# Kernel optimization log

Hardware: AMD Instinct MI355X
Metric: run time of the kernel (lower is better)

Reference implementation:

```python
import jax, jax.numpy as jnp
import numpy as np

D = 128
H = 8
B = 4
L = 2048


def setup_inputs() -> dict:
    key = jax.random.key(0)
    ks = jax.random.split(key, 5)
    s = 1.0 / np.sqrt(D)
    x = jax.random.normal(ks[0], (B, L, D), dtype=jnp.float32)
    Wq = jax.random.normal(ks[1], (D, D * H), dtype=jnp.float32) * s
    Wk = jax.random.normal(ks[2], (D, D * H), dtype=jnp.float32) * s
    Wv = jax.random.normal(ks[3], (D, D * H), dtype=jnp.float32) * s
    Wu = jax.random.normal(ks[4], (D * H, D), dtype=jnp.float32) * (1.0 / np.sqrt(D * H))
    bu = jnp.zeros((D,), dtype=jnp.float32)
    return {"x": x, "Wq": Wq, "Wk": Wk, "Wv": Wv, "Wu": Wu, "bu": bu}


def reference(x, Wq, Wk, Wv, Wu, bu):
    b, l, d = x.shape
    h = H
    # project and split heads: [b, l, h, d] -> [b, h, l, d]
    q = (x @ Wq).reshape(b, l, h, d).transpose(0, 2, 1, 3)
    k = (x @ Wk).reshape(b, l, h, d).transpose(0, 2, 1, 3)
    v = (x @ Wv).reshape(b, l, h, d).transpose(0, 2, 1, 3)
    scores = jnp.einsum("bhqd,bhkd->bhqk", q, k) / jnp.sqrt(jnp.float32(d))
    w = jax.nn.softmax(scores, axis=-1)
    out = jnp.einsum("bhqk,bhkd->bhqd", w, v)  # [b, h, l, d]
    out = out.transpose(0, 2, 1, 3).reshape(b, l, h * d)
    return out @ Wu + bu
```

## Files before the change

### kernel.cpp

```cpp
#include <hip/hip_runtime.h>
#include <stdint.h>

#define D_ 128
#define H_ 8
#define B_ 4
#define L_ 2048
#define NH (B_*H_)

typedef __bf16 bf16x8 __attribute__((ext_vector_type(8)));
typedef float f32x4 __attribute__((ext_vector_type(4)));
typedef float f32x16 __attribute__((ext_vector_type(16)));
typedef unsigned short u16;
typedef u16 u16x2 __attribute__((ext_vector_type(2)));
typedef u16 u16x4 __attribute__((ext_vector_type(4)));
typedef u16 u16x8 __attribute__((ext_vector_type(8)));
typedef uint32_t u32x2 __attribute__((ext_vector_type(2)));
typedef uint32_t u32x4 __attribute__((ext_vector_type(4)));
typedef float fvec4 __attribute__((ext_vector_type(4)));

__device__ __forceinline__ u16 f2b(float f){
    uint32_t u = __builtin_bit_cast(uint32_t, f);
    u += 0x7fffu + ((u >> 16) & 1u);
    return (u16)(u >> 16);
}
__device__ __forceinline__ u16 f2b_native(float f){
    return __builtin_bit_cast(u16, (__bf16)f);
}
__device__ __forceinline__ uint32_t pk2(float a, float b){
    u16x2 v = { f2b_native(a), f2b_native(b) };
    return __builtin_bit_cast(uint32_t, v);
}
__device__ __forceinline__ float ex2(float x){
#if __has_builtin(__builtin_amdgcn_exp2f)
    return __builtin_amdgcn_exp2f(x);
#else
    return exp2f(x);
#endif
}
__device__ __forceinline__ u32x2 permswap(uint32_t a, uint32_t b){
#if __has_builtin(__builtin_amdgcn_permlane32_swap)
    return __builtin_amdgcn_permlane32_swap(a, b, false, false);
#else
    asm volatile("v_permlane32_swap_b32 %0, %1" : "+v"(a), "+v"(b));
    u32x2 r; r[0] = a; r[1] = b; return r;
#endif
}
__device__ __forceinline__ bf16x8 asbf(u16x8 v){ return __builtin_bit_cast(bf16x8, v); }
#define MFMA(a,b,c)   __builtin_amdgcn_mfma_f32_16x16x32_bf16((a),(b),(c),0,0,0)
#define MFMA32(a,b,c) __builtin_amdgcn_mfma_f32_32x32x16_bf16((a),(b),(c),0,0,0)

__device__ __forceinline__ void gld16(const u16* g, u16* l){
    __builtin_amdgcn_global_load_lds(
        (const __attribute__((address_space(1))) void*)g,
        (__attribute__((address_space(3))) void*)l, 16, 0, 0);
}

__global__ __launch_bounds__(256)
void cvt_all(const float* __restrict__ x, const float* __restrict__ Wq,
             const float* __restrict__ Wk, const float* __restrict__ Wv,
             const float* __restrict__ Wu,
             u16* __restrict__ xb, u16* __restrict__ wT, u16* __restrict__ wuT)
{
    const int blk = blockIdx.x;
    const int t = threadIdx.x;
    if (blk < 512){
        size_t i = ((size_t)blk*256 + t)*8;
        fvec4 lo = *(const fvec4*)&x[i];
        fvec4 hi = *(const fvec4*)&x[i+4];
        u16x8 u;
        for (int j=0;j<4;++j){ u[j]=f2b(lo[j]); u[4+j]=f2b(hi[j]); }
        *(u16x8*)&xb[i] = u;
        return;
    }
    __shared__ __align__(16) u16 T[128][144];
    const int b = blk - 512;
    const float* src; int ld, coff, roff; u16* dst;
    if (b < 24){
        int mat = b>>3, head = b&7;
        src = (mat==0)?Wq:((mat==1)?Wk:Wv); ld = D_*H_; coff = head*128; roff = 0;
        dst = wT + (size_t)b*16384;
    } else {
        src = Wu; ld = D_; coff = 0; roff = (b-24)*128;
        dst = wuT + (size_t)(b-24)*16384;
    }
    for (int it=0; it<16; ++it){
        int k = it*8 + (t>>5), n0 = (t&31)*4;
        fvec4 wv = *(const fvec4*)&src[(size_t)(roff+k)*ld + coff + n0];
        for (int i=0;i<4;++i) T[n0+i][k] = f2b(wv[i]);
    }
    __syncthreads();
    for (int it=0; it<8; ++it){
        int gi = it*256 + t; int n = gi>>4, g = gi&15;
        *(u16x8*)&dst[n*128 + g*8] = *(const u16x8*)&T[n][(g^(n&7))*8];
    }
}

__global__ __launch_bounds__(256)
void qkv_proj(const u16* __restrict__ xb, const u16* __restrict__ wT,
              u16* __restrict__ q_ws, u16* __restrict__ k_ws, u16* __restrict__ v_ws)
{
    const int head = blockIdx.x;
    const int rt   = blockIdx.y;
    const int mat  = blockIdx.z;

    __shared__ __align__(16) u16 Xs[128*128];
    __shared__ __align__(16) u16 Ws[128*128];

    const int t = threadIdx.x;
    const int row0 = rt*128;
    const u16* wsrc = wT + (size_t)(mat*8 + head)*16384;

    for (int it=0; it<8; ++it){
        int gi = it*256 + t;
        int r = gi>>4, g = gi&15;
        gld16(&xb[(size_t)(row0+r)*D_ + ((g ^ (r&7))*8)], &Xs[(it*256 + (t>>6)*64)*8]);
        gld16(&wsrc[gi*8],                                &Ws[(it*256 + (t>>6)*64)*8]);
    }
    asm volatile("s_waitcnt vmcnt(0)" ::: "memory");
    __builtin_amdgcn_s_barrier();

    const int wave = t>>6, lane = t&63;
    const int wr = wave>>1, wc = wave&1;
    const int lrow = lane&15, lgrp = lane>>4;
    const int swz = lrow&7;

    f32x4 acc[4][4] = {};
    #pragma unroll
    for (int kc=0;kc<4;++kc){
        const int gd = kc*4 + lgrp;
        bf16x8 a[4], bfr[4];
        #pragma unroll
        for (int mr=0;mr<4;++mr)
            a[mr] = asbf(*(const u16x8*)&Xs[(wr*64+mr*16+lrow)*128 + ((gd ^ swz)*8)]);
        #pragma unroll
        for (int nr=0;nr<4;++nr)
            bfr[nr] = asbf(*(const u16x8*)&Ws[(wc*64+nr*16+lrow)*128 + ((gd ^ swz)*8)]);
        #pragma unroll
        for (int mr=0;mr<4;++mr)
            #pragma unroll
            for (int nr=0;nr<4;++nr)
                acc[mr][nr] = MFMA(a[mr], bfr[nr], acc[mr][nr]);
    }

    const float qscale = 0.12751879455370425f;
    for (int mr=0;mr<4;++mr){
        for (int nr=0;nr<4;++nr){
            f32x4 v = acc[mr][nr];
            int baserow = row0 + wr*64 + mr*16 + lgrp*4;
            int cd = wc*64 + nr*16 + lrow;
            int b  = baserow / L_;
            int l  = baserow % L_;
            int bh = b*H_ + head;
            if (mat==2){
                u16x4 pv;
                for (int r=0;r<4;++r) pv[r] = f2b(v[r]);
                size_t va = (size_t)bh*D_*L_ + (size_t)(l>>6)*8192 + ((l&63)>>3)*1024 + cd*8 + (l&7);
                *(u16x4*)&v_ws[va] = pv;
            } else if (mat==1){
                for (int r=0;r<4;++r){
                    int l2 = l + r;
                    size_t ka = (size_t)bh*L_*D_ + (size_t)(l2>>6)*8192 + (cd>>3)*512 + (l2&63)*8 + (cd&7);
                    k_ws[ka] = f2b(v[r]);
                }
            } else {
                for (int r=0;r<4;++r)
                    q_ws[((size_t)bh*L_ + (l + r))*D_ + cd] = f2b(v[r]*qscale);
            }
        }
    }
}

__global__ __launch_bounds__(512)
void attn(const u16* __restrict__ q_ws, const u16* __restrict__ k_ws,
          const u16* __restrict__ v_ws, u16* __restrict__ o_ws)
{
    const int wg = ((blockIdx.x & 7) << 5) | (blockIdx.x >> 3);
    const int qt = wg & 7;
    const int bh = wg >> 3;

    const int t = threadIdx.x, wave = t>>6, lane = t&63;
    const int q31 = lane & 31;
    const int hi  = lane >> 5;

    __shared__ __align__(16) u16 Kb[4][64*128];
    __shared__ __align__(16) u16 Vb[4][128*64];

    const int q0 = qt*256 + wave*32;

    bf16x8 qf[8];
    #pragma unroll
    for (int ks=0; ks<8; ++ks)
        qf[ks] = asbf(*(const u16x8*)&q_ws[((size_t)bh*L_ + q0 + q31)*D_ + ks*16 + hi*8]);

    const u16* kp = k_ws + (size_t)bh*L_*D_;
    const u16* vp = v_ws + (size_t)bh*D_*L_;

    auto stage = [&](int buf){
        #pragma unroll
        for (int i=0;i<2;++i){
            gld16(kp + (i*512 + t)*8, &Kb[buf][(i*512 + wave*64)*8]);
            gld16(vp + (i*512 + t)*8, &Vb[buf][(i*512 + wave*64)*8]);
        }
        kp += 8192;
        vp += 8192;
    };

    auto qkt = [&](int buf, f32x16& S0, f32x16& S1){
        f32x16 s0a = {}, s0b = {}, s1a = {}, s1b = {};
        #pragma unroll
        for (int ks=0; ks<4; ++ks){
            const int g0 = ks*2+hi, g1 = (ks+4)*2+hi;
            bf16x8 ka0 = asbf(*(const u16x8*)&Kb[buf][g0*512 + q31*8]);
            bf16x8 ka1 = asbf(*(const u16x8*)&Kb[buf][g1*512 + q31*8]);
            bf16x8 kb0 = asbf(*(const u16x8*)&Kb[buf][g0*512 + (32+q31)*8]);
            bf16x8 kb1 = asbf(*(const u16x8*)&Kb[buf][g1*512 + (32+q31)*8]);
            s0a = MFMA32(ka0, qf[ks],   s0a);
            s0b = MFMA32(ka1, qf[ks+4], s0b);
            s1a = MFMA32(kb0, qf[ks],   s1a);
            s1b = MFMA32(kb1, qf[ks+4], s1b);
        }
        S0 = s0a + s0b;
        S1 = s1a + s1b;
    };

    float lsA = 0.f, lsB = 0.f;
    f32x16 o4[4] = {};

    stage(0);
    stage(1);
    asm volatile("s_waitcnt vmcnt(0)" ::: "memory");
    __builtin_amdgcn_s_barrier();

    #define SM_PV(SREG, KS, BUF) do { \
        float p0 = ex2(SREG[((KS&1)*8)+0]); \
        float p1 = ex2(SREG[((KS&1)*8)+1]); \
        float p2 = ex2(SREG[((KS&1)*8)+2]); \
        float p3 = ex2(SREG[((KS&1)*8)+3]); \
        float p4 = ex2(SREG[((KS&1)*8)+4]); \
        float p5 = ex2(SREG[((KS&1)*8)+5]); \
        float p6 = ex2(SREG[((KS&1)*8)+6]); \
        float p7 = ex2(SREG[((KS&1)*8)+7]); \
        lsA += (p0+p1)+(p2+p3); \
        lsB += (p4+p5)+(p6+p7); \
        uint32_t cA = pk2(p0,p1), cB = pk2(p2,p3); \
        uint32_t cC = pk2(p4,p5), cD = pk2(p6,p7); \
        u32x2 r0 = permswap(cA, cC); \
        u32x2 r1 = permswap(cB, cD); \
        u32x4 wv; \
        wv[0] = r0[0];  wv[1] = r1[0]; \
        wv[2] = r0[1];  wv[3] = r1[1]; \
        bf16x8 pa = __builtin_bit_cast(bf16x8, wv); \
        __builtin_amdgcn_s_setprio(1); \
        _Pragma("unroll") \
        for (int nc2=0; nc2<4; ++nc2){ \
            bf16x8 vb = asbf(*(const u16x8*)&Vb[BUF][ (KS*2+hi)*1024 + (nc2*32+q31)*8 ]); \
            o4[nc2] = MFMA32(pa, vb, o4[nc2]); \
        } \
        __builtin_amdgcn_s_setprio(0); \
    } while(0)

    const int NJ = L_/128;
    for (int j=0; j<NJ; ++j){
        const int sa = (2*j) & 3, sb = (2*j+1) & 3;
        if (j < NJ-1){
            stage((2*j+2) & 3);
            stage((2*j+3) & 3);
        }

        f32x16 sA0, sA1;
        __builtin_amdgcn_s_setprio(1);
        qkt(sa, sA0, sA1);
        __builtin_amdgcn_s_setprio(0);
        SM_PV(sA0, 0, sa);
        SM_PV(sA0, 1, sa);
        SM_PV(sA1, 2, sa);
        SM_PV(sA1, 3, sa);

        f32x16 sB0, sB1;
        __builtin_amdgcn_s_setprio(1);
        qkt(sb, sB0, sB1);
        __builtin_amdgcn_s_setprio(0);
        SM_PV(sB0, 0, sb);
        SM_PV(sB0, 1, sb);
        SM_PV(sB1, 2, sb);
        SM_PV(sB1, 3, sb);

        if (j < NJ-1){
            asm volatile("s_waitcnt vmcnt(0)" ::: "memory");
            __builtin_amdgcn_s_barrier();
        }
    }
    #undef SM_PV

    float lsum = lsA + lsB;
    lsum += __shfl_xor(lsum, 32, 64);
    float inv = 1.0f / lsum;

    const int b = bh / H_, h = bh % H_;
    #pragma unroll
    for (int m=0; m<4; ++m){
        #pragma unroll
        for (int i=0; i<4; ++i){
            const int reg = m*4 + i;
            const int row = i + 8*m + 4*hi;
            float riv = __shfl(inv, row, 64);
            const int l = q0 + row;
            size_t base = ((size_t)(b*L_ + l))*(D_*H_) + h*128 + q31;
            #pragma unroll
            for (int nc2=0; nc2<4; ++nc2)
                o_ws[base + nc2*32] = f2b_native(o4[nc2][reg] * riv);
        }
    }
}

__global__ __launch_bounds__(256)
void out_proj(const u16* __restrict__ o_ws, const u16* __restrict__ wuT,
              const float* __restrict__ bu, float* __restrict__ out)
{
    const int rt = blockIdx.x;
    const int t = threadIdx.x, wave = t>>6, lane = t&63;
    const int wr = wave>>1, wc = wave&1;
    const int lrow = lane&15, lgrp = lane>>4;
    const int swz = lrow&7;

    __shared__ __align__(16) u16 As[2][32*128];
    __shared__ __align__(16) u16 Ws[2][128*128];

    const int row0 = rt*32;
    f32x4 acc[4] = {};

    auto stage = [&](int ks){
        const int buf = ks & 1;
        int gi = t;
        int r = gi>>4, g = gi&15;
        gld16(&o_ws[(size_t)(row0+r)*(D_*H_) + ks*128 + ((g ^ (r&7))*8)], &As[buf][((t>>6)*64)*8]);
        gi = 256 + t;
        r = gi>>4; g = gi&15;
        gld16(&o_ws[(size_t)(row0+r)*(D_*H_) + ks*128 + ((g ^ (r&7))*8)], &As[buf][(256 + (t>>6)*64)*8]);
        const u16* wsrc = wuT + (size_t)ks*16384;
        #pragma unroll
        for (int it=0; it<8; ++it)
            gld16(&wsrc[(it*256 + t)*8], &Ws[buf][(it*256 + (t>>6)*64)*8]);
    };

    stage(0);
    for (int ks=0; ks<8; ++ks){
        const int buf = ks & 1;
        if (ks < 7){
            stage(ks+1);
            asm volatile("s_waitcnt vmcnt(10)" ::: "memory");
        } else {
            asm volatile("s_waitcnt vmcnt(0)" ::: "memory");
        }
        __builtin_amdgcn_s_barrier();

        #pragma unroll
        for (int kc=0;kc<4;++kc){
            const int gd = kc*4 + lgrp;
            bf16x8 a = asbf(*(const u16x8*)&As[buf][(wr*16+lrow)*128 + ((gd ^ swz)*8)]);
            #pragma unroll
            for (int nc=0;nc<4;++nc){
                bf16x8 b = asbf(*(const u16x8*)&Ws[buf][(wc*64+nc*16+lrow)*128 + ((gd ^ swz)*8)]);
                acc[nc] = MFMA(a, b, acc[nc]);
            }
        }
        __builtin_amdgcn_s_barrier();
    }

    for (int nc=0;nc<4;++nc){
        for (int r=0;r<4;++r){
            int row = row0 + wr*16 + lgrp*4 + r;
            int n = wc*64 + nc*16 + lrow;
            out[(size_t)row*D_ + n] = acc[nc][r] + bu[n];
        }
    }
}

extern "C" void kernel_launch(void* const* d_in, const int* in_sizes, int n_in,
                              void* d_out, int out_size, void* d_ws, size_t ws_size,
                              hipStream_t stream)
{
    const float* x  = (const float*)d_in[0];
    const float* Wq = (const float*)d_in[1];
    const float* Wk = (const float*)d_in[2];
    const float* Wv = (const float*)d_in[3];
    const float* Wu = (const float*)d_in[4];
    const float* bu = (const float*)d_in[5];
    float* out = (float*)d_out;

    u16* ws = (u16*)d_ws;
    const size_t SZ = (size_t)NH * L_ * D_;
    u16* q_ws = ws;
    u16* k_ws = q_ws + SZ;
    u16* v_ws = k_ws + SZ;
    u16* o_ws = v_ws + SZ;
    u16* x_bf = o_ws + SZ;
    u16* wT   = x_bf + (size_t)B_*L_*D_;
    u16* wuT  = wT + 24*16384;

    cvt_all<<<dim3(544), 256, 0, stream>>>(x, Wq, Wk, Wv, Wu, x_bf, wT, wuT);
    qkv_proj<<<dim3(H_, (B_*L_)/128, 3), 256, 0, stream>>>(x_bf, wT, q_ws, k_ws, v_ws);
    attn<<<dim3((L_/256)*NH), 512, 0, stream>>>(q_ws, k_ws, v_ws, o_ws);
    out_proj<<<dim3((B_*L_)/32), 256, 0, stream>>>(o_ws, wuT, bu, out);
}
```

Before: 119.0 us.

## Give each attention wave 64 query rows to reuse K/V fragments

The attention kernel now runs 4 waves of 256 threads instead of 8 waves, and each wave handles two 32-row query tiles. Each K fragment and V fragment loaded from LDS then feeds two MFMAs, which halves LDS read traffic per MFMA. Staging loops double their iteration count to cover the same tile with fewer threads. The cost is roughly doubled accumulator and Q register pressure and half as many waves per workgroup to hide latency.

```diff
diff --git a/kernel.cpp b/kernel.cpp
--- a/kernel.cpp
+++ b/kernel.cpp
@@ -170,7 +170,7 @@
     }
 }
 
-__global__ __launch_bounds__(512)
+__global__ __launch_bounds__(256, 1)
 void attn(const u16* __restrict__ q_ws, const u16* __restrict__ k_ws,
           const u16* __restrict__ v_ws, u16* __restrict__ o_ws)
 {
@@ -185,76 +185,74 @@
     __shared__ __align__(16) u16 Kb[4][64*128];
     __shared__ __align__(16) u16 Vb[4][128*64];
 
-    const int q0 = qt*256 + wave*32;
-
-    bf16x8 qf[8];
+    const int q0 = qt*256 + wave*64;
+
+    bf16x8 qfA[8], qfB[8];
     #pragma unroll
-    for (int ks=0; ks<8; ++ks)
-        qf[ks] = asbf(*(const u16x8*)&q_ws[((size_t)bh*L_ + q0 + q31)*D_ + ks*16 + hi*8]);
+    for (int ks=0; ks<8; ++ks){
+        qfA[ks] = asbf(*(const u16x8*)&q_ws[((size_t)bh*L_ + q0      + q31)*D_ + ks*16 + hi*8]);
+        qfB[ks] = asbf(*(const u16x8*)&q_ws[((size_t)bh*L_ + q0 + 32 + q31)*D_ + ks*16 + hi*8]);
+    }
 
     const u16* kp = k_ws + (size_t)bh*L_*D_;
     const u16* vp = v_ws + (size_t)bh*D_*L_;
 
     auto stage = [&](int buf){
         #pragma unroll
-        for (int i=0;i<2;++i){
-            gld16(kp + (i*512 + t)*8, &Kb[buf][(i*512 + wave*64)*8]);
-            gld16(vp + (i*512 + t)*8, &Vb[buf][(i*512 + wave*64)*8]);
+        for (int i=0;i<4;++i){
+            gld16(kp + (i*256 + t)*8, &Kb[buf][(i*256 + wave*64)*8]);
+            gld16(vp + (i*256 + t)*8, &Vb[buf][(i*256 + wave*64)*8]);
         }
         kp += 8192;
         vp += 8192;
     };
 
-    auto qkt = [&](int buf, f32x16& S0, f32x16& S1){
-        f32x16 s0a = {}, s0b = {}, s1a = {}, s1b = {};
-        #pragma unroll
-        for (int ks=0; ks<4; ++ks){
-            const int g0 = ks*2+hi, g1 = (ks+4)*2+hi;
-            bf16x8 ka0 = asbf(*(const u16x8*)&Kb[buf][g0*512 + q31*8]);
-            bf16x8 ka1 = asbf(*(const u16x8*)&Kb[buf][g1*512 + q31*8]);
-            bf16x8 kb0 = asbf(*(const u16x8*)&Kb[buf][g0*512 + (32+q31)*8]);
-            bf16x8 kb1 = asbf(*(const u16x8*)&Kb[buf][g1*512 + (32+q31)*8]);
-            s0a = MFMA32(ka0, qf[ks],   s0a);
-            s0b = MFMA32(ka1, qf[ks+4], s0b);
-            s1a = MFMA32(kb0, qf[ks],   s1a);
-            s1b = MFMA32(kb1, qf[ks+4], s1b);
-        }
-        S0 = s0a + s0b;
-        S1 = s1a + s1b;
+    auto qkt = [&](int buf, f32x16& SA0, f32x16& SA1, f32x16& SB0, f32x16& SB1){
+        f32x16 sA0 = {}, sA1 = {}, sB0 = {}, sB1 = {};
+        #pragma unroll
+        for (int ks=0; ks<8; ++ks){
+            const int g = ks*2 + hi;
+            bf16x8 ka = asbf(*(const u16x8*)&Kb[buf][g*512 + q31*8]);
+            bf16x8 kb = asbf(*(const u16x8*)&Kb[buf][g*512 + (32+q31)*8]);
+            sA0 = MFMA32(ka, qfA[ks], sA0);
+            sB0 = MFMA32(ka, qfB[ks], sB0);
+            sA1 = MFMA32(kb, qfA[ks], sA1);
+            sB1 = MFMA32(kb, qfB[ks], sB1);
+        }
+        SA0 = sA0; SA1 = sA1; SB0 = sB0; SB1 = sB1;
     };
 
-    float lsA = 0.f, lsB = 0.f;
-    f32x16 o4[4] = {};
+    float lsA_A = 0.f, lsB_A = 0.f, lsA_B = 0.f, lsB_B = 0.f;
+    f32x16 oA[4] = {}, oB[4] = {};
 
     stage(0);
     stage(1);
     asm volatile("s_waitcnt vmcnt(0)" ::: "memory");
     __builtin_amdgcn_s_barrier();
 
-    #define SM_PV(SREG, KS, BUF) do { \
-        float p0 = ex2(SREG[((KS&1)*8)+0]); \
-        float p1 = ex2(SREG[((KS&1)*8)+1]); \
-        float p2 = ex2(SREG[((KS&1)*8)+2]); \
-        float p3 = ex2(SREG[((KS&1)*8)+3]); \
-        float p4 = ex2(SREG[((KS&1)*8)+4]); \
-        float p5 = ex2(SREG[((KS&1)*8)+5]); \
-        float p6 = ex2(SREG[((KS&1)*8)+6]); \
-        float p7 = ex2(SREG[((KS&1)*8)+7]); \
-        lsA += (p0+p1)+(p2+p3); \
-        lsB += (p4+p5)+(p6+p7); \
-        uint32_t cA = pk2(p0,p1), cB = pk2(p2,p3); \
-        uint32_t cC = pk2(p4,p5), cD = pk2(p6,p7); \
-        u32x2 r0 = permswap(cA, cC); \
-        u32x2 r1 = permswap(cB, cD); \
-        u32x4 wv; \
-        wv[0] = r0[0];  wv[1] = r1[0]; \
-        wv[2] = r0[1];  wv[3] = r1[1]; \
-        bf16x8 pa = __builtin_bit_cast(bf16x8, wv); \
+    #define SM_PV2(SA, SB, KS, BUF) do { \
+        const int h = (KS&1)*8; \
+        float a0 = ex2(SA[h+0]), a1 = ex2(SA[h+1]), a2 = ex2(SA[h+2]), a3 = ex2(SA[h+3]); \
+        float a4 = ex2(SA[h+4]), a5 = ex2(SA[h+5]), a6 = ex2(SA[h+6]), a7 = ex2(SA[h+7]); \
+        float b0 = ex2(SB[h+0]), b1 = ex2(SB[h+1]), b2 = ex2(SB[h+2]), b3 = ex2(SB[h+3]); \
+        float b4 = ex2(SB[h+4]), b5 = ex2(SB[h+5]), b6 = ex2(SB[h+6]), b7 = ex2(SB[h+7]); \
+        lsA_A += (a0+a1)+(a2+a3);  lsB_A += (a4+a5)+(a6+a7); \
+        lsA_B += (b0+b1)+(b2+b3);  lsB_B += (b4+b5)+(b6+b7); \
+        uint32_t cA0 = pk2(a0,a1), cA1 = pk2(a2,a3), cA2 = pk2(a4,a5), cA3 = pk2(a6,a7); \
+        uint32_t cB0 = pk2(b0,b1), cB1 = pk2(b2,b3), cB2 = pk2(b4,b5), cB3 = pk2(b6,b7); \
+        u32x2 rA0 = permswap(cA0, cA2), rA1 = permswap(cA1, cA3); \
+        u32x2 rB0 = permswap(cB0, cB2), rB1 = permswap(cB1, cB3); \
+        u32x4 wvA, wvB; \
+        wvA[0]=rA0[0]; wvA[1]=rA1[0]; wvA[2]=rA0[1]; wvA[3]=rA1[1]; \
+        wvB[0]=rB0[0]; wvB[1]=rB1[0]; wvB[2]=rB0[1]; wvB[3]=rB1[1]; \
+        bf16x8 paA = __builtin_bit_cast(bf16x8, wvA); \
+        bf16x8 paB = __builtin_bit_cast(bf16x8, wvB); \
         __builtin_amdgcn_s_setprio(1); \
         _Pragma("unroll") \
         for (int nc2=0; nc2<4; ++nc2){ \
             bf16x8 vb = asbf(*(const u16x8*)&Vb[BUF][ (KS*2+hi)*1024 + (nc2*32+q31)*8 ]); \
-            o4[nc2] = MFMA32(pa, vb, o4[nc2]); \
+            oA[nc2] = MFMA32(paA, vb, oA[nc2]); \
+            oB[nc2] = MFMA32(paB, vb, oB[nc2]); \
         } \
         __builtin_amdgcn_s_setprio(0); \
     } while(0)
@@ -267,34 +265,36 @@
             stage((2*j+3) & 3);
         }
 
-        f32x16 sA0, sA1;
+        f32x16 sA0, sA1, sB0, sB1;
         __builtin_amdgcn_s_setprio(1);
-        qkt(sa, sA0, sA1);
+        qkt(sa, sA0, sA1, sB0, sB1);
         __builtin_amdgcn_s_setprio(0);
-        SM_PV(sA0, 0, sa);
-        SM_PV(sA0, 1, sa);
-        SM_PV(sA1, 2, sa);
-        SM_PV(sA1, 3, sa);
-
-        f32x16 sB0, sB1;
+        SM_PV2(sA0, sB0, 0, sa);
+        SM_PV2(sA0, sB0, 1, sa);
+        SM_PV2(sA1, sB1, 2, sa);
+        SM_PV2(sA1, sB1, 3, sa);
+
         __builtin_amdgcn_s_setprio(1);
-        qkt(sb, sB0, sB1);
+        qkt(sb, sA0, sA1, sB0, sB1);
         __builtin_amdgcn_s_setprio(0);
-        SM_PV(sB0, 0, sb);
-        SM_PV(sB0, 1, sb);
-        SM_PV(sB1, 2, sb);
-        SM_PV(sB1, 3, sb);
+        SM_PV2(sA0, sB0, 0, sb);
+        SM_PV2(sA0, sB0, 1, sb);
+        SM_PV2(sA1, sB1, 2, sb);
+        SM_PV2(sA1, sB1, 3, sb);
 
         if (j < NJ-1){
             asm volatile("s_waitcnt vmcnt(0)" ::: "memory");
             __builtin_amdgcn_s_barrier();
         }
     }
-    #undef SM_PV
-
-    float lsum = lsA + lsB;
-    lsum += __shfl_xor(lsum, 32, 64);
-    float inv = 1.0f / lsum;
+    #undef SM_PV2
+
+    float lsumA = lsA_A + lsB_A;
+    float lsumB = lsA_B + lsB_B;
+    lsumA += __shfl_xor(lsumA, 32, 64);
+    lsumB += __shfl_xor(lsumB, 32, 64);
+    float invA = 1.0f / lsumA;
+    float invB = 1.0f / lsumB;
 
     const int b = bh / H_, h = bh % H_;
     #pragma unroll
@@ -303,12 +303,15 @@
         for (int i=0; i<4; ++i){
             const int reg = m*4 + i;
             const int row = i + 8*m + 4*hi;
-            float riv = __shfl(inv, row, 64);
-            const int l = q0 + row;
-            size_t base = ((size_t)(b*L_ + l))*(D_*H_) + h*128 + q31;
+            float rivA = __shfl(invA, row, 64);
+            float rivB = __shfl(invB, row, 64);
+            size_t baseA = ((size_t)(b*L_ + q0 + row))*(D_*H_) + h*128 + q31;
+            size_t baseB = ((size_t)(b*L_ + q0 + 32 + row))*(D_*H_) + h*128 + q31;
             #pragma unroll
-            for (int nc2=0; nc2<4; ++nc2)
-                o_ws[base + nc2*32] = f2b_native(o4[nc2][reg] * riv);
+            for (int nc2=0; nc2<4; ++nc2){
+                o_ws[baseA + nc2*32] = f2b_native(oA[nc2][reg] * rivA);
+                o_ws[baseB + nc2*32] = f2b_native(oB[nc2][reg] * rivB);
+            }
         }
     }
 }
@@ -400,6 +403,6 @@
 
     cvt_all<<<dim3(544), 256, 0, stream>>>(x, Wq, Wk, Wv, Wu, x_bf, wT, wuT);
     qkv_proj<<<dim3(H_, (B_*L_)/128, 3), 256, 0, stream>>>(x_bf, wT, q_ws, k_ws, v_ws);
-    attn<<<dim3((L_/256)*NH), 512, 0, stream>>>(q_ws, k_ws, v_ws, o_ws);
+    attn<<<dim3((L_/256)*NH), 256, 0, stream>>>(q_ws, k_ws, v_ws, o_ws);
     out_proj<<<dim3((B_*L_)/32), 256, 0, stream>>>(o_ws, wuT, bu, out);
 }
```

New measurement: 123.6 us. 3.8% more time.

## Process two row tiles per QKV block with double-buffered X prefetch

Applied to the files above, without the earlier changes.

Each qkv_proj block now handles two 128-row tiles, reusing one weight tile load and prefetching the second X tile into a second LDS buffer while the first tile's MFMAs run. The grid shrinks from 1536 to 768 blocks. This cuts redundant weight loads and hides some global-load latency. In exchange, LDS use per block rises to 96KB, which can lower occupancy, and there is less block-level parallelism.

```diff
diff --git a/kernel.cpp b/kernel.cpp
--- a/kernel.cpp
+++ b/kernel.cpp
@@ -99,72 +99,89 @@
 void qkv_proj(const u16* __restrict__ xb, const u16* __restrict__ wT,
               u16* __restrict__ q_ws, u16* __restrict__ k_ws, u16* __restrict__ v_ws)
 {
-    const int head = blockIdx.x;
-    const int rt   = blockIdx.y;
-    const int mat  = blockIdx.z;
-
-    __shared__ __align__(16) u16 Xs[128*128];
+    const int head = blockIdx.x & 7;
+    const int mat  = blockIdx.x >> 3;
+    const int rtg  = blockIdx.y;
+
+    __shared__ __align__(16) u16 Xs[2][128*128];
     __shared__ __align__(16) u16 Ws[128*128];
 
     const int t = threadIdx.x;
-    const int row0 = rt*128;
     const u16* wsrc = wT + (size_t)(mat*8 + head)*16384;
 
-    for (int it=0; it<8; ++it){
-        int gi = it*256 + t;
-        int r = gi>>4, g = gi&15;
-        gld16(&xb[(size_t)(row0+r)*D_ + ((g ^ (r&7))*8)], &Xs[(it*256 + (t>>6)*64)*8]);
-        gld16(&wsrc[gi*8],                                &Ws[(it*256 + (t>>6)*64)*8]);
-    }
+    auto stageX = [&](int buf, int row0){
+        #pragma unroll
+        for (int it=0; it<8; ++it){
+            int gi = it*256 + t;
+            int r = gi>>4, g = gi&15;
+            gld16(&xb[(size_t)(row0+r)*D_ + ((g ^ (r&7))*8)], &Xs[buf][(it*256 + (t>>6)*64)*8]);
+        }
+    };
+
+    for (int it=0; it<8; ++it)
+        gld16(&wsrc[(it*256 + t)*8], &Ws[(it*256 + (t>>6)*64)*8]);
+    stageX(0, (rtg*2)*128);
     asm volatile("s_waitcnt vmcnt(0)" ::: "memory");
     __builtin_amdgcn_s_barrier();
+
+    stageX(1, (rtg*2+1)*128);
 
     const int wave = t>>6, lane = t&63;
     const int wr = wave>>1, wc = wave&1;
     const int lrow = lane&15, lgrp = lane>>4;
     const int swz = lrow&7;
-
-    f32x4 acc[4][4] = {};
+    const float qscale = 0.12751879455370425f;
+
     #pragma unroll
-    for (int kc=0;kc<4;++kc){
-        const int gd = kc*4 + lgrp;
-        bf16x8 a[4], bfr[4];
-        #pragma unroll
-        for (int mr=0;mr<4;++mr)
-            a[mr] = asbf(*(const u16x8*)&Xs[(wr*64+mr*16+lrow)*128 + ((gd ^ swz)*8)]);
-        #pragma unroll
-        for (int nr=0;nr<4;++nr)
-            bfr[nr] = asbf(*(const u16x8*)&Ws[(wc*64+nr*16+lrow)*128 + ((gd ^ swz)*8)]);
-        #pragma unroll
-        for (int mr=0;mr<4;++mr)
+    for (int tt=0; tt<2; ++tt){
+        const int row0 = (rtg*2+tt)*128;
+
+        f32x4 acc[4][4] = {};
+        #pragma unroll
+        for (int kc=0;kc<4;++kc){
+            const int gd = kc*4 + lgrp;
+            bf16x8 a[4], bfr[4];
+            #pragma unroll
+            for (int mr=0;mr<4;++mr)
+                a[mr] = asbf(*(const u16x8*)&Xs[tt][(wr*64+mr*16+lrow)*128 + ((gd ^ swz)*8)]);
             #pragma unroll
             for (int nr=0;nr<4;++nr)
-                acc[mr][nr] = MFMA(a[mr], bfr[nr], acc[mr][nr]);
-    }
-
-    const float qscale = 0.12751879455370425f;
-    for (int mr=0;mr<4;++mr){
-        for (int nr=0;nr<4;++nr){
-            f32x4 v = acc[mr][nr];
-            int baserow = row0 + wr*64 + mr*16 + lgrp*4;
-            int cd = wc*64 + nr*16 + lrow;
-            int b  = baserow / L_;
-            int l  = baserow % L_;
-            int bh = b*H_ + head;
-            if (mat==2){
-                u16x4 pv;
-                for (int r=0;r<4;++r) pv[r] = f2b(v[r]);
-                size_t va = (size_t)bh*D_*L_ + (size_t)(l>>6)*8192 + ((l&63)>>3)*1024 + cd*8 + (l&7);
-                *(u16x4*)&v_ws[va] = pv;
-            } else if (mat==1){
-                for (int r=0;r<4;++r){
-                    int l2 = l + r;
-                    size_t ka = (size_t)bh*L_*D_ + (size_t)(l2>>6)*8192 + (cd>>3)*512 + (l2&63)*8 + (cd&7);
-                    k_ws[ka] = f2b(v[r]);
+                bfr[nr] = asbf(*(const u16x8*)&Ws[(wc*64+nr*16+lrow)*128 + ((gd ^ swz)*8)]);
+            #pragma unroll
+            for (int mr=0;mr<4;++mr)
+                #pragma unroll
+                for (int nr=0;nr<4;++nr)
+                    acc[mr][nr] = MFMA(a[mr], bfr[nr], acc[mr][nr]);
+        }
+
+        if (tt == 0){
+            asm volatile("s_waitcnt vmcnt(0)" ::: "memory");
+            __builtin_amdgcn_s_barrier();
+        }
+
+        for (int mr=0;mr<4;++mr){
+            for (int nr=0;nr<4;++nr){
+                f32x4 v = acc[mr][nr];
+                int baserow = row0 + wr*64 + mr*16 + lgrp*4;
+                int cd = wc*64 + nr*16 + lrow;
+                int b  = baserow / L_;
+                int l  = baserow % L_;
+                int bh = b*H_ + head;
+                if (mat==2){
+                    u16x4 pv;
+                    for (int r=0;r<4;++r) pv[r] = f2b(v[r]);
+                    size_t va = (size_t)bh*D_*L_ + (size_t)(l>>6)*8192 + ((l&63)>>3)*1024 + cd*8 + (l&7);
+                    *(u16x4*)&v_ws[va] = pv;
+                } else if (mat==1){
+                    for (int r=0;r<4;++r){
+                        int l2 = l + r;
+                        size_t ka = (size_t)bh*L_*D_ + (size_t)(l2>>6)*8192 + (cd>>3)*512 + (l2&63)*8 + (cd&7);
+                        k_ws[ka] = f2b(v[r]);
+                    }
+                } else {
+                    for (int r=0;r<4;++r)
+                        q_ws[((size_t)bh*L_ + (l + r))*D_ + cd] = f2b(v[r]*qscale);
                 }
-            } else {
-                for (int r=0;r<4;++r)
-                    q_ws[((size_t)bh*L_ + (l + r))*D_ + cd] = f2b(v[r]*qscale);
             }
         }
     }
@@ -399,7 +416,7 @@
     u16* wuT  = wT + 24*16384;
 
     cvt_all<<<dim3(544), 256, 0, stream>>>(x, Wq, Wk, Wv, Wu, x_bf, wT, wuT);
-    qkv_proj<<<dim3(H_, (B_*L_)/128, 3), 256, 0, stream>>>(x_bf, wT, q_ws, k_ws, v_ws);
+    qkv_proj<<<dim3(24, 32), 256, 0, stream>>>(x_bf, wT, q_ws, k_ws, v_ws);
     attn<<<dim3((L_/256)*NH), 512, 0, stream>>>(q_ws, k_ws, v_ws, o_ws);
     out_proj<<<dim3((B_*L_)/32), 256, 0, stream>>>(o_ws, wuT, bu, out);
 }
```

Result: slower. 123.7 us (+3.9%).
